# Performance work log

Hardware: AMD Instinct MI355X
Metric: run time of the kernel (lower is better)

Reference implementation:

```python
import jax, jax.numpy as jnp
import numpy as np

N = 10000       # nodes
E = 160000      # edges
D_IN = 256      # in_channels (node feature dim)
H1, C = 8, 32   # conv1: 8 heads x 32 -> 256; conv2: 1 head x 32
MSG = 128       # msg_dim
TD = 128        # time encoder out_channels
ED = MSG + TD   # edge_dim = 256
HC1 = H1 * C    # 256


def _lin(key, shape, scale=0.05):
    return jax.random.normal(key, shape, dtype=jnp.float32) * scale


def setup_inputs() -> dict:
    key = jax.random.key(0)
    ks = jax.random.split(key, 32)
    inp = {}
    inp["x"] = jax.random.normal(ks[0], (N, D_IN), dtype=jnp.float32)
    inp["last_update"] = jax.random.uniform(ks[1], (N,), jnp.float32, 0.0, 1000.0)
    inp["edge_index"] = jax.random.randint(ks[2], (2, E), 0, N)
    inp["t"] = jax.random.uniform(ks[3], (E,), jnp.float32, 0.0, 1000.0)
    inp["msg"] = jax.random.normal(ks[4], (E, MSG), dtype=jnp.float32)
    # TimeEncoder: Linear(1, TD) then cos
    inp["time_w"] = _lin(ks[5], (TD, 1), 0.1)
    inp["time_b"] = jnp.zeros((TD,), jnp.float32)
    # conv1 (TransformerConv in=256, heads=8, per-head 32, edge_dim=256, concat=True)
    inp["Wq1"] = _lin(ks[6], (D_IN, HC1)); inp["bq1"] = jnp.zeros((HC1,), jnp.float32)
    inp["Wk1"] = _lin(ks[7], (D_IN, HC1)); inp["bk1"] = jnp.zeros((HC1,), jnp.float32)
    inp["Wv1"] = _lin(ks[8], (D_IN, HC1)); inp["bv1"] = jnp.zeros((HC1,), jnp.float32)
    inp["We1"] = _lin(ks[9], (ED, HC1))   # lin_edge has no bias in PyG
    inp["Ws1"] = _lin(ks[10], (D_IN, HC1)); inp["bs1"] = jnp.zeros((HC1,), jnp.float32)
    # conv2 (in=256, heads=1, per-head 32, concat=False)
    inp["Wq2"] = _lin(ks[11], (HC1, C)); inp["bq2"] = jnp.zeros((C,), jnp.float32)
    inp["Wk2"] = _lin(ks[12], (HC1, C)); inp["bk2"] = jnp.zeros((C,), jnp.float32)
    inp["Wv2"] = _lin(ks[13], (HC1, C)); inp["bv2"] = jnp.zeros((C,), jnp.float32)
    inp["We2"] = _lin(ks[14], (ED, C))
    inp["Ws2"] = _lin(ks[15], (HC1, C)); inp["bs2"] = jnp.zeros((C,), jnp.float32)
    return inp


def transformer_conv(x, src, dst, edge_attr, Wq, bq, Wk, bk, Wv, bv, We, Ws, bs, heads, ch, concat):
    n = x.shape[0]
    q = (x @ Wq + bq).reshape(n, heads, ch)
    k = (x @ Wk + bk).reshape(n, heads, ch)
    v = (x @ Wv + bv).reshape(n, heads, ch)
    e = (edge_attr @ We).reshape(-1, heads, ch)       # [E,H,C]
    ke = k[src] + e                                    # key_j + edge
    ve = v[src] + e                                    # value_j + edge
    alpha = jnp.einsum('ehc,ehc->eh', q[dst], ke) / jnp.sqrt(jnp.float32(ch))
    # segment softmax over incoming edges of each destination node
    amax = jax.ops.segment_max(alpha, dst, num_segments=n)   # -inf for empty segs
    ex = jnp.exp(alpha - amax[dst])
    den = jax.ops.segment_sum(ex, dst, num_segments=n)
    attn = ex / (den[dst] + 1e-16)                     # [E,H]
    out = jax.ops.segment_sum(attn[:, :, None] * ve, dst, num_segments=n)  # [N,H,C]
    out = out.reshape(n, heads * ch) if concat else out.mean(axis=1)
    return out + (x @ Ws + bs)                         # root skip connection


def reference(x, last_update, edge_index, t, msg, time_w, time_b,
              Wq1, bq1, Wk1, bk1, Wv1, bv1, We1, Ws1, bs1,
              Wq2, bq2, Wk2, bk2, Wv2, bv2, We2, Ws2, bs2):
    src, dst = edge_index[0], edge_index[1]
    rel_t = last_update[src] - t                       # [E]
    rel_t_enc = jnp.cos(rel_t[:, None] * time_w[:, 0][None, :] + time_b)  # [E,TD]
    edge_attr = jnp.concatenate([rel_t_enc, msg], axis=-1)                # [E,ED]
    h = jax.nn.relu(transformer_conv(x, src, dst, edge_attr,
                                     Wq1, bq1, Wk1, bk1, Wv1, bv1, We1, Ws1, bs1,
                                     H1, C, True))
    out = jax.nn.relu(transformer_conv(h, src, dst, edge_attr,
                                       Wq2, bq2, Wk2, bk2, Wv2, bv2, We2, Ws2, bs2,
                                       1, C, False))
    return out
```

## Files before the change

kernel.cpp:

```cpp
#include <hip/hip_runtime.h>
#include <math.h>

#define N_NODES 10000
#define N_EDGES 160000
#define RT1 157
#define RTE 2500
#define CONVX_T (RT1 * 64 * 32)
#define MAXSEG 16
#define SEGSTRIDE 576

static inline int ceildiv(int a, int b) { return (a + b - 1) / b; }

typedef float f32x4 __attribute__((ext_vector_type(4)));
typedef short bf16x8 __attribute__((ext_vector_type(8)));

__device__ __forceinline__ unsigned short f2bf(float f) {
  unsigned int u = __builtin_bit_cast(unsigned int, f);
  u += 0x7FFFu + ((u >> 16) & 1u);
  return (unsigned short)(u >> 16);
}
__device__ __forceinline__ float bf2f(unsigned short h) {
  unsigned int u = ((unsigned int)h) << 16;
  return __builtin_bit_cast(float, u);
}

__global__ void count_kernel(const int* __restrict__ dstp, int* __restrict__ deg, int E) {
  for (int i = blockIdx.x * blockDim.x + threadIdx.x; i < E; i += gridDim.x * blockDim.x)
    atomicAdd(&deg[dstp[i]], 1);
}

__global__ void scan_kernel(const int* __restrict__ deg, int* __restrict__ rowptr, int n) {
  __shared__ int part[1024];
  const int tid = threadIdx.x;
  const int CHK = 10;
  int base = tid * CHK;
  int loc[CHK];
  int s = 0;
#pragma unroll
  for (int j = 0; j < CHK; ++j) {
    int idx = base + j;
    int v = (idx < n) ? deg[idx] : 0;
    loc[j] = s; s += v;
  }
  part[tid] = s;
  __syncthreads();
  for (int off = 1; off < 1024; off <<= 1) {
    int y = (tid >= off) ? part[tid - off] : 0;
    __syncthreads();
    part[tid] += y;
    __syncthreads();
  }
  int pre = tid ? part[tid - 1] : 0;
#pragma unroll
  for (int j = 0; j < CHK; ++j) {
    int idx = base + j;
    if (idx < n) rowptr[idx] = pre + loc[j];
  }
  if (tid == 1023) rowptr[n] = part[1023];
}

__global__ void scatter_kernel(const float* __restrict__ lu, const float* __restrict__ tt,
                               const int* __restrict__ srcp, const int* __restrict__ dstp,
                               const int* __restrict__ rowptr, int* __restrict__ fill,
                               int* __restrict__ srcs, int* __restrict__ dsts,
                               int* __restrict__ eidA, float* __restrict__ rel_s, int E) {
  for (int e = blockIdx.x * blockDim.x + threadIdx.x; e < E; e += gridDim.x * blockDim.x) {
    int d = dstp[e], s = srcp[e];
    int pos = atomicAdd(&fill[d], 1);
    int slot = rowptr[d] + pos;
    srcs[slot] = s;
    dsts[slot] = d;
    eidA[slot] = e;
    rel_s[slot] = lu[s] - tt[e];
  }
}

__device__ __forceinline__ void wstore(const float* __restrict__ W, unsigned short* __restrict__ out,
                                       int Nin, int n_off, int NFtot, int k, int c) {
  int gc = n_off + c;
  int ks=k>>5, kg=(k>>3)&3, j=k&7, nf=gc>>4, ic=gc&15;
  out[(size_t)(ks*NFtot+nf)*512 + (ic+16*kg)*8 + j] = f2bf(W[(size_t)k*Nin + c]);
}

__global__ void conv_all_kernel(const float* __restrict__ x, unsigned short* __restrict__ xa,
                                const float* Wq1, const float* Wk1, const float* Wv1, const float* Ws1,
                                const float* We1, const float* Wq2, const float* Wk2, const float* Wv2,
                                const float* Ws2, const float* We2,
                                const float* bq1, const float* bk1, const float* bv1, const float* bs1,
                                const float* bq2, const float* bk2, const float* bv2, const float* bs2,
                                unsigned short* W1f, unsigned short* We1f, unsigned short* W2f,
                                unsigned short* We2f, float* bcat1, float* bcat2) {
  int t0 = blockIdx.x * blockDim.x + threadIdx.x;
  if (t0 < CONVX_T) {
    int i = t0 >> 5, k8 = t0 & 31;
    union { uint4 q; unsigned short s[8]; } u;
    if (i < N_NODES) {
      const float4* px = (const float4*)(x + (size_t)i * 256 + k8 * 8);
      float4 f0 = px[0], f1 = px[1];
      u.s[0]=f2bf(f0.x); u.s[1]=f2bf(f0.y); u.s[2]=f2bf(f0.z); u.s[3]=f2bf(f0.w);
      u.s[4]=f2bf(f1.x); u.s[5]=f2bf(f1.y); u.s[6]=f2bf(f1.z); u.s[7]=f2bf(f1.w);
    } else {
      u.q = make_uint4(0,0,0,0);
    }
    int rt=i>>6, rf=(i>>4)&3, ir=i&15, ks=k8>>2, kg=k8&3;
    *(uint4*)&xa[(size_t)rt*16384 + ks*2048 + rf*512 + (ir+16*kg)*8] = u.q;
    return;
  }
  int t = t0 - CONVX_T;
  if (t < 262144) {
    int w = t >> 16, r = t & 65535, k = r >> 8, c = r & 255;
    const float* W = (w == 0) ? Wq1 : (w == 1) ? Wk1 : (w == 2) ? Wv1 : Ws1;
    wstore(W, W1f, 256, w * 256, 64, k, c);
  } else if (t < 327680) {
    int r = t - 262144, k = r >> 8, c = r & 255;
    wstore(We1, We1f, 256, 0, 16, k, c);
  } else if (t < 360448) {
    int r = t - 327680, w = r >> 13, r2 = r & 8191, k = r2 >> 5, c = r2 & 31;
    const float* W = (w == 0) ? Wq2 : (w == 1) ? Wk2 : (w == 2) ? Wv2 : Ws2;
    wstore(W, W2f, 32, w * 32, 8, k, c);
  } else if (t < 368640) {
    int r = t - 360448, k = r >> 5, c = r & 31;
    wstore(We2, We2f, 32, 0, 4, k, c);
  } else if (t < 369792) {
    int r = t - 368640;
    if (r < 1024) {
      const float* b = (r < 256) ? bq1 : (r < 512) ? bk1 : (r < 768) ? bv1 : bs1;
      bcat1[r] = b[r & 255];
    } else {
      int r2 = r - 1024;
      const float* b = (r2 < 32) ? bq2 : (r2 < 64) ? bk2 : (r2 < 96) ? bv2 : bs2;
      bcat2[r2] = b[r2 & 31];
    }
  }
}

__global__ __launch_bounds__(512, 4)
void node1_gemm(const unsigned short* __restrict__ xa, const unsigned short* __restrict__ W1f,
                const float* __restrict__ bcat1, float* __restrict__ qf,
                unsigned short* __restrict__ kvb, float* __restrict__ sf) {
  __shared__ char ldsraw[32768];
  uint4* lds4 = (uint4*)ldsraw;
  const int tid = threadIdx.x;
  const int wid = tid >> 6, lane = tid & 63;
  const int fr0 = (lane >> 4) * 4;
  const int fc0 = lane & 15;
  const int rt0 = blockIdx.x % RT1;
  const int y = blockIdx.x / RT1;
  const int phase = rt0 & 7;

#pragma unroll
  for (int s = 0; s < 4; ++s)
    lds4[tid + s * 512] = *(const uint4*)(xa + (size_t)rt0 * 16384 + (size_t)(tid + s * 512) * 8);
  __syncthreads();

  f32x4 acc[4][2];
#pragma unroll
  for (int i = 0; i < 4; ++i)
#pragma unroll
    for (int j = 0; j < 2; ++j) acc[i][j] = (f32x4){0.f, 0.f, 0.f, 0.f};

  bf16x8 aN0, aN1, aN2, aN3, bN0, bN1;
  {
    const int ks = phase;
    aN0 = *(const bf16x8*)&lds4[ks * 256 + 0 * 64 + lane];
    aN1 = *(const bf16x8*)&lds4[ks * 256 + 1 * 64 + lane];
    aN2 = *(const bf16x8*)&lds4[ks * 256 + 2 * 64 + lane];
    aN3 = *(const bf16x8*)&lds4[ks * 256 + 3 * 64 + lane];
    bN0 = *(const bf16x8*)(W1f + ((size_t)(ks * 64 + y * 16 + wid * 2 + 0)) * 512 + (size_t)lane * 8);
    bN1 = *(const bf16x8*)(W1f + ((size_t)(ks * 64 + y * 16 + wid * 2 + 1)) * 512 + (size_t)lane * 8);
  }
#pragma unroll
  for (int ksi = 0; ksi < 8; ++ksi) {
    bf16x8 aC0 = aN0, aC1 = aN1, aC2 = aN2, aC3 = aN3;
    bf16x8 bC0 = bN0, bC1 = bN1;
    if (ksi < 7) {
      const int ks2 = (ksi + 1) ^ phase;
      aN0 = *(const bf16x8*)&lds4[ks2 * 256 + 0 * 64 + lane];
      aN1 = *(const bf16x8*)&lds4[ks2 * 256 + 1 * 64 + lane];
      aN2 = *(const bf16x8*)&lds4[ks2 * 256 + 2 * 64 + lane];
      aN3 = *(const bf16x8*)&lds4[ks2 * 256 + 3 * 64 + lane];
      bN0 = *(const bf16x8*)(W1f + ((size_t)(ks2 * 64 + y * 16 + wid * 2 + 0)) * 512 + (size_t)lane * 8);
      bN1 = *(const bf16x8*)(W1f + ((size_t)(ks2 * 64 + y * 16 + wid * 2 + 1)) * 512 + (size_t)lane * 8);
    }
    acc[0][0] = __builtin_amdgcn_mfma_f32_16x16x32_bf16(aC0, bC0, acc[0][0], 0, 0, 0);
    acc[1][0] = __builtin_amdgcn_mfma_f32_16x16x32_bf16(aC1, bC0, acc[1][0], 0, 0, 0);
    acc[2][0] = __builtin_amdgcn_mfma_f32_16x16x32_bf16(aC2, bC0, acc[2][0], 0, 0, 0);
    acc[3][0] = __builtin_amdgcn_mfma_f32_16x16x32_bf16(aC3, bC0, acc[3][0], 0, 0, 0);
    acc[0][1] = __builtin_amdgcn_mfma_f32_16x16x32_bf16(aC0, bC1, acc[0][1], 0, 0, 0);
    acc[1][1] = __builtin_amdgcn_mfma_f32_16x16x32_bf16(aC1, bC1, acc[1][1], 0, 0, 0);
    acc[2][1] = __builtin_amdgcn_mfma_f32_16x16x32_bf16(aC2, bC1, acc[2][1], 0, 0, 0);
    acc[3][1] = __builtin_amdgcn_mfma_f32_16x16x32_bf16(aC3, bC1, acc[3][1], 0, 0, 0);
  }

  bool bf16path;
  void* dstp_; int cstr_, dc0_, bcol0_;
  if (y == 0)      { bf16path = false; dstp_ = qf;  cstr_ = 256; dc0_ = 0;   bcol0_ = 0; }
  else if (y == 1) { bf16path = true;  dstp_ = kvb; cstr_ = 512; dc0_ = 0;   bcol0_ = 256; }
  else if (y == 2) { bf16path = true;  dstp_ = kvb; cstr_ = 512; dc0_ = 256; bcol0_ = 512; }
  else             { bf16path = false; dstp_ = sf;  cstr_ = 256; dc0_ = 0;   bcol0_ = 768; }
  if (!bf16path) {
    float* dst = (float*)dstp_;
    const int row0 = rt0 * 64 + fr0;
#pragma unroll
    for (int cf = 0; cf < 2; ++cf) {
      int c = wid * 32 + cf * 16 + fc0;
      float bv = bcat1[bcol0_ + c];
#pragma unroll
      for (int rf = 0; rf < 4; ++rf) {
#pragma unroll
        for (int j = 0; j < 4; ++j) {
          int r = row0 + rf * 16 + j;
          if (r < N_NODES) dst[(size_t)r * cstr_ + c] = acc[rf][cf][j] + bv;
        }
      }
    }
  } else {
    __syncthreads();
    unsigned short* cl = (unsigned short*)ldsraw;
    unsigned short* dst = (unsigned short*)dstp_;
    for (int pass = 0; pass < 4; ++pass) {
      if ((wid >> 1) == pass) {
#pragma unroll
        for (int cf = 0; cf < 2; ++cf) {
          int c = (wid & 1) * 32 + cf * 16 + fc0;
          float bv = bcat1[bcol0_ + pass * 64 + c];
#pragma unroll
          for (int rf = 0; rf < 4; ++rf)
#pragma unroll
            for (int j = 0; j < 4; ++j)
              cl[(fr0 + rf * 16 + j) * 72 + c] = f2bf(acc[rf][cf][j] + bv);
        }
      }
      __syncthreads();
      {
        int row = tid >> 3, cc = (tid & 7) * 8;
        int gr = rt0 * 64 + row;
        if (gr < N_NODES)
          *(uint4*)&dst[(size_t)gr * cstr_ + dc0_ + pass * 64 + cc] = *(const uint4*)&cl[row * 72 + cc];
      }
      __syncthreads();
    }
  }
}

__global__ __launch_bounds__(512, 4)
void edge_fused(const float* __restrict__ qf, const unsigned short* __restrict__ kvb,
                const unsigned short* __restrict__ We1f, const unsigned short* __restrict__ We2f,
                char* __restrict__ segrec, unsigned short* __restrict__ e2b,
                const float* __restrict__ rel_s, const float* __restrict__ tw,
                const float* __restrict__ tb, const float* __restrict__ msg,
                const int* __restrict__ eidA, const int* __restrict__ srcsA,
                const int* __restrict__ dstsA, const int* __restrict__ rowptr) {
  __shared__ char ldsraw[38912];
  uint4* lds4 = (uint4*)ldsraw;
  unsigned short* e1t = (unsigned short*)ldsraw;
  int* dseg     = (int*)(ldsraw + 33280);
  int* sseg     = (int*)(ldsraw + 33536);
  unsigned short* cl2 = (unsigned short*)(ldsraw + 33792);

  const int tid = threadIdx.x;
  const int wid = tid >> 6, lane = tid & 63;
  const int bx = blockIdx.x;
  const int fr0 = (lane >> 4) * 4;
  const int fc0 = lane & 15;
  const int rt0 = bx;
  const int phase = bx & 7;

  {
    const int rem = tid & 255;
    const int ksh = tid >> 8;
    const int arf = rem >> 6, ar2 = rem & 63, air = ar2 & 15, akg = ar2 >> 4;
    const int slot = rt0 * 64 + arf * 16 + air;
    float rl = rel_s[slot];
    int eorg = eidA[slot];
#pragma unroll
    for (int s = 0; s < 2; ++s) {
      int ks = ksh + s * 2;
      int k8 = ks * 4 + akg;
      const float4* twp = (const float4*)(tw + k8 * 8);
      const float4* tbp = (const float4*)(tb + k8 * 8);
      float4 w0 = twp[0], w1 = twp[1], b0 = tbp[0], b1 = tbp[1];
      union { uint4 q; unsigned short us[8]; } u;
      u.us[0]=f2bf(__cosf(rl*w0.x+b0.x)); u.us[1]=f2bf(__cosf(rl*w0.y+b0.y));
      u.us[2]=f2bf(__cosf(rl*w0.z+b0.z)); u.us[3]=f2bf(__cosf(rl*w0.w+b0.w));
      u.us[4]=f2bf(__cosf(rl*w1.x+b1.x)); u.us[5]=f2bf(__cosf(rl*w1.y+b1.y));
      u.us[6]=f2bf(__cosf(rl*w1.z+b1.z)); u.us[7]=f2bf(__cosf(rl*w1.w+b1.w));
      lds4[ks * 256 + rem] = u.q;
    }
#pragma unroll
    for (int s = 0; s < 2; ++s) {
      int ks = 4 + ksh + s * 2;
      int k8 = ks * 4 + akg;
      const float4* pm = (const float4*)(msg + (size_t)eorg * 128 + (size_t)(k8 - 16) * 8);
      float4 f0 = pm[0], f1 = pm[1];
      union { uint4 q; unsigned short us[8]; } u;
      u.us[0]=f2bf(f0.x); u.us[1]=f2bf(f0.y); u.us[2]=f2bf(f0.z); u.us[3]=f2bf(f0.w);
      u.us[4]=f2bf(f1.x); u.us[5]=f2bf(f1.y); u.us[6]=f2bf(f1.z); u.us[7]=f2bf(f1.w);
      lds4[ks * 256 + rem] = u.q;
    }
  }
  __syncthreads();

  f32x4 acc[4][2];
  f32x4 acc2[4];
#pragma unroll
  for (int i = 0; i < 4; ++i) {
    acc2[i] = (f32x4){0.f, 0.f, 0.f, 0.f};
#pragma unroll
    for (int j = 0; j < 2; ++j) acc[i][j] = (f32x4){0.f, 0.f, 0.f, 0.f};
  }

  bf16x8 aN0, aN1, aN2, aN3, bN0, bN1, b2N;
  {
    const int ks = phase;
    aN0 = *(const bf16x8*)&lds4[ks * 256 + 0 * 64 + lane];
    aN1 = *(const bf16x8*)&lds4[ks * 256 + 1 * 64 + lane];
    aN2 = *(const bf16x8*)&lds4[ks * 256 + 2 * 64 + lane];
    aN3 = *(const bf16x8*)&lds4[ks * 256 + 3 * 64 + lane];
    bN0 = *(const bf16x8*)(We1f + ((size_t)(ks * 16 + wid * 2 + 0)) * 512 + (size_t)lane * 8);
    bN1 = *(const bf16x8*)(We1f + ((size_t)(ks * 16 + wid * 2 + 1)) * 512 + (size_t)lane * 8);
    b2N = 0;
    if (wid < 2) b2N = *(const bf16x8*)(We2f + ((size_t)(ks * 4 + wid)) * 512 + (size_t)lane * 8);
  }
#pragma unroll
  for (int ksi = 0; ksi < 8; ++ksi) {
    bf16x8 aC0 = aN0, aC1 = aN1, aC2 = aN2, aC3 = aN3;
    bf16x8 bC0 = bN0, bC1 = bN1, b2C = b2N;
    if (ksi < 7) {
      const int ks2 = (ksi + 1) ^ phase;
      aN0 = *(const bf16x8*)&lds4[ks2 * 256 + 0 * 64 + lane];
      aN1 = *(const bf16x8*)&lds4[ks2 * 256 + 1 * 64 + lane];
      aN2 = *(const bf16x8*)&lds4[ks2 * 256 + 2 * 64 + lane];
      aN3 = *(const bf16x8*)&lds4[ks2 * 256 + 3 * 64 + lane];
      bN0 = *(const bf16x8*)(We1f + ((size_t)(ks2 * 16 + wid * 2 + 0)) * 512 + (size_t)lane * 8);
      bN1 = *(const bf16x8*)(We1f + ((size_t)(ks2 * 16 + wid * 2 + 1)) * 512 + (size_t)lane * 8);
      if (wid < 2) b2N = *(const bf16x8*)(We2f + ((size_t)(ks2 * 4 + wid)) * 512 + (size_t)lane * 8);
    }
    acc[0][0] = __builtin_amdgcn_mfma_f32_16x16x32_bf16(aC0, bC0, acc[0][0], 0, 0, 0);
    acc[1][0] = __builtin_amdgcn_mfma_f32_16x16x32_bf16(aC1, bC0, acc[1][0], 0, 0, 0);
    acc[2][0] = __builtin_amdgcn_mfma_f32_16x16x32_bf16(aC2, bC0, acc[2][0], 0, 0, 0);
    acc[3][0] = __builtin_amdgcn_mfma_f32_16x16x32_bf16(aC3, bC0, acc[3][0], 0, 0, 0);
    acc[0][1] = __builtin_amdgcn_mfma_f32_16x16x32_bf16(aC0, bC1, acc[0][1], 0, 0, 0);
    acc[1][1] = __builtin_amdgcn_mfma_f32_16x16x32_bf16(aC1, bC1, acc[1][1], 0, 0, 0);
    acc[2][1] = __builtin_amdgcn_mfma_f32_16x16x32_bf16(aC2, bC1, acc[2][1], 0, 0, 0);
    acc[3][1] = __builtin_amdgcn_mfma_f32_16x16x32_bf16(aC3, bC1, acc[3][1], 0, 0, 0);
    if (wid < 2) {
      acc2[0] = __builtin_amdgcn_mfma_f32_16x16x32_bf16(aC0, b2C, acc2[0], 0, 0, 0);
      acc2[1] = __builtin_amdgcn_mfma_f32_16x16x32_bf16(aC1, b2C, acc2[1], 0, 0, 0);
      acc2[2] = __builtin_amdgcn_mfma_f32_16x16x32_bf16(aC2, b2C, acc2[2], 0, 0, 0);
      acc2[3] = __builtin_amdgcn_mfma_f32_16x16x32_bf16(aC3, b2C, acc2[3], 0, 0, 0);
    }
  }

  __syncthreads();
  if (tid < 64) {
    dseg[tid] = dstsA[rt0 * 64 + tid];
    sseg[tid] = srcsA[rt0 * 64 + tid];
  }
#pragma unroll
  for (int cf = 0; cf < 2; ++cf)
#pragma unroll
    for (int rf = 0; rf < 4; ++rf)
#pragma unroll
      for (int j = 0; j < 4; ++j)
        e1t[(fr0 + rf * 16 + j) * 260 + wid * 32 + cf * 16 + fc0] = f2bf(acc[rf][cf][j]);
  if (wid < 2) {
#pragma unroll
    for (int rf = 0; rf < 4; ++rf)
#pragma unroll
      for (int j = 0; j < 4; ++j)
        cl2[(fr0 + rf * 16 + j) * 40 + wid * 16 + fc0] = f2bf(acc2[rf][j]);
  }
  __syncthreads();

  if (tid < 256) {
    int row = tid >> 2, cc = (tid & 3) * 8;
    *(uint4*)&e2b[(size_t)(rt0 * 64 + row) * 32 + cc] = *(const uint4*)&cl2[row * 40 + cc];
  }

  {
    const int base = wid * 8;
    const int rgj = bx * 8 + wid;
    int d8[8], s8[8];
#pragma unroll
    for (int t = 0; t < 8; ++t) { d8[t] = dseg[base + t]; s8[t] = sseg[base + t]; }

    float4 q8[8]; ushort4 k8[8], e8[8];
#pragma unroll
    for (int t = 0; t < 8; ++t) {
      q8[t] = *(const float4*)&qf[(size_t)d8[t] * 256 + lane * 4];
      k8[t] = *(const ushort4*)&kvb[(size_t)s8[t] * 512 + lane * 4];
      e8[t] = *(const ushort4*)&e1t[(base + t) * 260 + lane * 4];
    }
    float sc[8];
#pragma unroll
    for (int t = 0; t < 8; ++t) {
      float p = q8[t].x * (bf2f(k8[t].x) + bf2f(e8[t].x))
              + q8[t].y * (bf2f(k8[t].y) + bf2f(e8[t].y))
              + q8[t].z * (bf2f(k8[t].z) + bf2f(e8[t].z))
              + q8[t].w * (bf2f(k8[t].w) + bf2f(e8[t].w));
      p += __shfl_xor(p, 1); p += __shfl_xor(p, 2); p += __shfl_xor(p, 4);
      sc[t] = p * 0.17677669529663687f;
    }
    ushort4 v8[8];
#pragma unroll
    for (int t = 0; t < 8; ++t)
      v8[t] = *(const ushort4*)&kvb[(size_t)s8[t] * 512 + 256 + lane * 4];

    float m8[8], w8[8];
#pragma unroll
    for (int t = 0; t < 8; ++t) {
      float mm = sc[t];
#pragma unroll
      for (int u = 0; u < 8; ++u)
        if (d8[u] == d8[t]) mm = fmaxf(mm, sc[u]);
      m8[t] = mm;
      w8[t] = __expf(sc[t] - mm);
    }
#pragma unroll
    for (int t = 0; t < 8; ++t) {
      bool first = (t == 0) || (d8[t - 1] != d8[t]);
      if (first && (lane & 7) == 0) {
        float den = 0.f;
#pragma unroll
        for (int u = 0; u < 8; ++u)
          if (d8[u] == d8[t]) den += w8[u];
        int j = rgj - (rowptr[d8[t]] >> 3);
        if (j < MAXSEG) {
          float* rec = (float*)(segrec + ((size_t)d8[t] * MAXSEG + j) * SEGSTRIDE);
          rec[128 + (lane >> 3)] = m8[t];
          rec[136 + (lane >> 3)] = den;
        }
      }
    }
    f32x4 pacc = (f32x4){0.f, 0.f, 0.f, 0.f};
    int cur = d8[0];
#pragma unroll
    for (int t = 0; t < 8; ++t) {
      if (d8[t] != cur) {
        int j = rgj - (rowptr[cur] >> 3);
        if (j < MAXSEG) {
          unsigned short* pp = (unsigned short*)(segrec + ((size_t)cur * MAXSEG + j) * SEGSTRIDE);
          ushort4 o;
          o.x = f2bf(pacc[0]); o.y = f2bf(pacc[1]); o.z = f2bf(pacc[2]); o.w = f2bf(pacc[3]);
          *(ushort4*)&pp[lane * 4] = o;
        }
        pacc = (f32x4){0.f, 0.f, 0.f, 0.f};
        cur = d8[t];
      }
      pacc[0] += w8[t] * (bf2f(v8[t].x) + bf2f(e8[t].x));
      pacc[1] += w8[t] * (bf2f(v8[t].y) + bf2f(e8[t].y));
      pacc[2] += w8[t] * (bf2f(v8[t].z) + bf2f(e8[t].z));
      pacc[3] += w8[t] * (bf2f(v8[t].w) + bf2f(e8[t].w));
    }
    {
      int j = rgj - (rowptr[cur] >> 3);
      if (j < MAXSEG) {
        unsigned short* pp = (unsigned short*)(segrec + ((size_t)cur * MAXSEG + j) * SEGSTRIDE);
        ushort4 o;
        o.x = f2bf(pacc[0]); o.y = f2bf(pacc[1]); o.z = f2bf(pacc[2]); o.w = f2bf(pacc[3]);
        *(ushort4*)&pp[lane * 4] = o;
      }
    }
  }
}

__global__ __launch_bounds__(64)
void merge_kernel(const char* __restrict__ segrec, const int* __restrict__ rowptr,
                  const float* __restrict__ sf, unsigned short* __restrict__ ha) {
  const int n = blockIdx.x;
  const int lane = threadIdx.x;
  const int beg = rowptr[n], end = rowptr[n + 1];
  const float4 sk = *(const float4*)&sf[(size_t)n * 256 + lane * 4];
  float o0, o1, o2, o3;
  if (beg == end) {
    o0 = sk.x; o1 = sk.y; o2 = sk.z; o3 = sk.w;
  } else {
    const int h = lane >> 3;
    int s0 = beg >> 3, s1 = (end - 1) >> 3;
    int span = s1 - s0 + 1; if (span > MAXSEG) span = MAXSEG;
    float M = -INFINITY;
    for (int j = 0; j < span; ++j) {
      const float* rec = (const float*)(segrec + ((size_t)n * MAXSEG + j) * SEGSTRIDE);
      M = fmaxf(M, rec[128 + h]);
    }
    float den = 0.f;
    f32x4 num = (f32x4){0.f, 0.f, 0.f, 0.f};
    for (int j = 0; j < span; ++j) {
      const float* rec = (const float*)(segrec + ((size_t)n * MAXSEG + j) * SEGSTRIDE);
      float sc = __expf(rec[128 + h] - M);
      den += sc * rec[136 + h];
      ushort4 p4 = *(const ushort4*)((const unsigned short*)rec + lane * 4);
      num[0] += sc * bf2f(p4.x); num[1] += sc * bf2f(p4.y);
      num[2] += sc * bf2f(p4.z); num[3] += sc * bf2f(p4.w);
    }
    const float inv = 1.f / (den + 1e-16f);
    o0 = num[0] * inv + sk.x; o1 = num[1] * inv + sk.y;
    o2 = num[2] * inv + sk.z; o3 = num[3] * inv + sk.w;
  }
  o0 = fmaxf(o0, 0.f); o1 = fmaxf(o1, 0.f); o2 = fmaxf(o2, 0.f); o3 = fmaxf(o3, 0.f);
  int rt = n >> 6, rf = (n >> 4) & 3, ir = n & 15;
  int h2 = lane >> 3;
  int kg = (lane & 7) >> 1, jj = 4 * (lane & 1);
  ushort4 w4;
  w4.x = f2bf(o0); w4.y = f2bf(o1); w4.z = f2bf(o2); w4.w = f2bf(o3);
  *(ushort4*)&ha[(size_t)rt * 16384 + h2 * 2048 + rf * 512 + (ir + 16 * kg) * 8 + jj] = w4;
}

__global__ __launch_bounds__(256)
void gemm_node2(const unsigned short* __restrict__ ha, const unsigned short* __restrict__ W2f,
                const float* __restrict__ bcat2, float* __restrict__ qkvs2) {
  const int tid = threadIdx.x;
  const int wid = tid >> 6, lane = tid & 63;
  const int wr = wid >> 1, wc = wid & 1;
  const int rt0 = blockIdx.x * 2;
  int rtA = rt0 + wr;
  if (rtA >= RT1) rtA = RT1 - 1;

  f32x4 acc[4][4];
#pragma unroll
  for (int i = 0; i < 4; ++i)
#pragma unroll
    for (int j = 0; j < 4; ++j) acc[i][j] = (f32x4){0.f, 0.f, 0.f, 0.f};

#pragma unroll
  for (int ks = 0; ks < 8; ++ks) {
    bf16x8 a[4], b[4];
#pragma unroll
    for (int rf = 0; rf < 4; ++rf)
      a[rf] = *(const bf16x8*)(ha + (size_t)rtA * 16384 + (size_t)ks * 2048 + (size_t)(rf * 64 + lane) * 8);
#pragma unroll
    for (int cf = 0; cf < 4; ++cf)
      b[cf] = *(const bf16x8*)(W2f + ((size_t)(ks * 8 + wc * 4 + cf)) * 512 + (size_t)lane * 8);
#pragma unroll
    for (int rf = 0; rf < 4; ++rf)
#pragma unroll
      for (int cf = 0; cf < 4; ++cf)
        acc[rf][cf] = __builtin_amdgcn_mfma_f32_16x16x32_bf16(a[rf], b[cf], acc[rf][cf], 0, 0, 0);
  }

  const int row0 = (rt0 + wr) * 64 + ((lane >> 4) * 4);
  const int cb2 = wc * 64 + (lane & 15);
#pragma unroll
  for (int cf = 0; cf < 4; ++cf) {
    int c = cb2 + cf * 16;
    float bv = bcat2[c];
#pragma unroll
    for (int rf = 0; rf < 4; ++rf) {
#pragma unroll
      for (int j = 0; j < 4; ++j) {
        int r = row0 + rf * 16 + j;
        if (r < N_NODES) qkvs2[(size_t)r * 128 + c] = acc[rf][cf][j] + bv;
      }
    }
  }
}

__global__ __launch_bounds__(64)
void attn2_kernel(const float* __restrict__ qkvs2, const unsigned short* __restrict__ e2b,
                  const int* __restrict__ srcs, const int* __restrict__ rowptr,
                  float* __restrict__ outp) {
  const int n = blockIdx.x;
  const int tid = threadIdx.x;
  const int c = tid & 31;
  const int beg = rowptr[n], end = rowptr[n + 1];
  const float qv = qkvs2[(size_t)n * 128 + c];

  float m0=-INFINITY,d0=0,x0=0;
  float m1=-INFINITY,d1=0,x1=0;
  float m2=-INFINITY,d2=0,x2=0;
  float m3=-INFINITY,d3=0,x3=0;

  auto step = [&](int i, float& m, float& d, float& a) {
    const int s = srcs[i];
    const float ev = bf2f(e2b[(size_t)i * 32 + c]);
    float p = qv * (qkvs2[(size_t)s * 128 + 32 + c] + ev);
    const float v = qkvs2[(size_t)s * 128 + 64 + c] + ev;
#pragma unroll
    for (int off = 16; off; off >>= 1) p += __shfl_xor(p, off);
    p *= 0.17677669529663687f;
    const float mn = fmaxf(m, p);
    const float sc = __expf(m - mn), w = __expf(p - mn);
    d = d * sc + w; a = a * sc + w * v; m = mn;
  };

  int i = beg;
  for (; i + 3 < end; i += 4) {
    step(i, m0, d0, x0);
    step(i + 1, m1, d1, x1);
    step(i + 2, m2, d2, x2);
    step(i + 3, m3, d3, x3);
  }
  for (; i < end; ++i) step(i, m0, d0, x0);

  auto merge = [&](float& m, float& d, float& a, float mB, float dB, float b) {
    if (mB == -INFINITY) return;
    const float M = fmaxf(m, mB);
    const float sA = __expf(m - M), sB = __expf(mB - M);
    d = d * sA + dB * sB; a = a * sA + b * sB; m = M;
  };
  merge(m0, d0, x0, m1, d1, x1);
  merge(m2, d2, x2, m3, d3, x3);
  merge(m0, d0, x0, m2, d2, x2);

  if (tid < 32) {
    float o = x0 / (d0 + 1e-16f) + qkvs2[(size_t)n * 128 + 96 + c];
    outp[(size_t)n * 32 + c] = fmaxf(o, 0.f);
  }
}

extern "C" void kernel_launch(void* const* d_in, const int* in_sizes, int n_in,
                              void* d_out, int out_size, void* d_ws, size_t ws_size,
                              hipStream_t stream) {
  const float* x   = (const float*)d_in[0];
  const float* lu  = (const float*)d_in[1];
  const int*   ei  = (const int*)d_in[2];
  const float* tt  = (const float*)d_in[3];
  const float* msg = (const float*)d_in[4];
  const float* tw  = (const float*)d_in[5];
  const float* tb  = (const float*)d_in[6];
  const float* Wq1 = (const float*)d_in[7];  const float* bq1 = (const float*)d_in[8];
  const float* Wk1 = (const float*)d_in[9];  const float* bk1 = (const float*)d_in[10];
  const float* Wv1 = (const float*)d_in[11]; const float* bv1 = (const float*)d_in[12];
  const float* We1 = (const float*)d_in[13];
  const float* Ws1 = (const float*)d_in[14]; const float* bs1 = (const float*)d_in[15];
  const float* Wq2 = (const float*)d_in[16]; const float* bq2 = (const float*)d_in[17];
  const float* Wk2 = (const float*)d_in[18]; const float* bk2 = (const float*)d_in[19];
  const float* Wv2 = (const float*)d_in[20]; const float* bv2 = (const float*)d_in[21];
  const float* We2 = (const float*)d_in[22];
  const float* Ws2 = (const float*)d_in[23]; const float* bs2 = (const float*)d_in[24];

  const int* srcp = ei;
  const int* dstp = ei + N_EDGES;

  char* p = (char*)d_ws;
  auto alloc = [&](size_t bytes) -> char* {
    char* r = p;
    p += (bytes + 255) & ~(size_t)255;
    return r;
  };
  int*   deg     = (int*)alloc((size_t)N_NODES * 4);
  int*   fill    = (int*)alloc((size_t)N_NODES * 4);
  int*   rowptr  = (int*)alloc((size_t)(N_NODES + 1) * 4);
  int*   srcs    = (int*)alloc((size_t)N_EDGES * 4);
  int*   dsts    = (int*)alloc((size_t)N_EDGES * 4);
  int*   eidA    = (int*)alloc((size_t)N_EDGES * 4);
  float* rel_s   = (float*)alloc((size_t)N_EDGES * 4);
  unsigned short* xa   = (unsigned short*)alloc((size_t)RT1 * 32768);
  unsigned short* W1f  = (unsigned short*)alloc((size_t)8 * 64 * 1024);
  unsigned short* We1f = (unsigned short*)alloc((size_t)8 * 16 * 1024);
  unsigned short* W2f  = (unsigned short*)alloc((size_t)8 * 8 * 1024);
  unsigned short* We2f = (unsigned short*)alloc((size_t)8 * 4 * 1024);
  float* bcat1  = (float*)alloc(1024 * 4);
  float* bcat2  = (float*)alloc(128 * 4);
  float* qf     = (float*)alloc((size_t)N_NODES * 256 * 4);
  unsigned short* kvb = (unsigned short*)alloc((size_t)N_NODES * 512 * 2);
  float* sf     = (float*)alloc((size_t)N_NODES * 256 * 4);
  char*  segrec = (char*)alloc((size_t)N_NODES * MAXSEG * SEGSTRIDE);
  unsigned short* ha  = (unsigned short*)alloc((size_t)RT1 * 32768);
  float* qkvs2  = (float*)alloc((size_t)N_NODES * 128 * 4);
  unsigned short* e2b = (unsigned short*)alloc((size_t)N_EDGES * 32 * 2);
  float* outp   = (float*)d_out;

  hipMemsetAsync(deg, 0, (size_t)N_NODES * 4, stream);
  hipMemsetAsync(fill, 0, (size_t)N_NODES * 4, stream);
  hipMemsetAsync(ha + (size_t)(RT1 - 1) * 16384, 0, 32768, stream);

  count_kernel<<<625, 256, 0, stream>>>(dstp, deg, N_EDGES);
  scan_kernel<<<1, 1024, 0, stream>>>(deg, rowptr, N_NODES);
  scatter_kernel<<<625, 256, 0, stream>>>(lu, tt, srcp, dstp, rowptr, fill,
                                          srcs, dsts, eidA, rel_s, N_EDGES);

  conv_all_kernel<<<ceildiv(CONVX_T + 369792, 256), 256, 0, stream>>>(
      x, xa, Wq1, Wk1, Wv1, Ws1, We1, Wq2, Wk2, Wv2, Ws2, We2,
      bq1, bk1, bv1, bs1, bq2, bk2, bv2, bs2,
      W1f, We1f, W2f, We2f, bcat1, bcat2);

  node1_gemm<<<RT1 * 4, 512, 0, stream>>>(xa, W1f, bcat1, qf, kvb, sf);

  edge_fused<<<RTE, 512, 0, stream>>>(
      qf, kvb, We1f, We2f, segrec, e2b,
      rel_s, tw, tb, msg, eidA, srcs, dsts, rowptr);

  merge_kernel<<<N_NODES, 64, 0, stream>>>(segrec, rowptr, sf, ha);
  gemm_node2<<<ceildiv(RT1, 2), 256, 0, stream>>>(ha, W2f, bcat2, qkvs2);
  attn2_kernel<<<N_NODES, 64, 0, stream>>>(qkvs2, e2b, srcs, rowptr, outp);
}
```

Measured before the change: 170.8 us.

## Fuse merge into node2 GEMM, overlap msg loads with cos compute, batch attn2 nodes

The separate merge_kernel and gemm_node2 are fused into node2_fused. It merges segment records per node and writes the bf16 A-tile straight into LDS, removing the global ha buffer, its memset and one launch. In edge_fused the msg loads are issued early and the first half of the K loop runs on the cos features, with the msg half converted and stored to LDS afterwards; this hides global load latency but adds a barrier and drops the phase-rotated K order. attn2 now packs four nodes per 256-thread block instead of one per 64-thread block. The fused node2 kernel has only 157 blocks with a serial per-thread merge loop, so it may run with low parallelism.

```diff
diff --git a/kernel.cpp b/kernel.cpp
--- a/kernel.cpp
+++ b/kernel.cpp
@@ -264,15 +264,23 @@
   const int fr0 = (lane >> 4) * 4;
   const int fc0 = lane & 15;
   const int rt0 = bx;
-  const int phase = bx & 7;
-
+
+  const int rem = tid & 255;
+  const int ksh = tid >> 8;
+  float4 mA0, mA1, mB0, mB1;
   {
-    const int rem = tid & 255;
-    const int ksh = tid >> 8;
     const int arf = rem >> 6, ar2 = rem & 63, air = ar2 & 15, akg = ar2 >> 4;
     const int slot = rt0 * 64 + arf * 16 + air;
+    int eorg = eidA[slot];
+    const float4* pmA = (const float4*)(msg + (size_t)eorg * 128 + (size_t)(ksh * 4 + akg) * 8);
+    mA0 = pmA[0]; mA1 = pmA[1];
+    const float4* pmB = (const float4*)(msg + (size_t)eorg * 128 + (size_t)((2 + ksh) * 4 + akg) * 8);
+    mB0 = pmB[0]; mB1 = pmB[1];
+    if (tid < 64) {
+      dseg[tid] = dstsA[rt0 * 64 + tid];
+      sseg[tid] = srcsA[rt0 * 64 + tid];
+    }
     float rl = rel_s[slot];
-    int eorg = eidA[slot];
 #pragma unroll
     for (int s = 0; s < 2; ++s) {
       int ks = ksh + s * 2;
@@ -287,17 +295,6 @@
       u.us[6]=f2bf(__cosf(rl*w1.z+b1.z)); u.us[7]=f2bf(__cosf(rl*w1.w+b1.w));
       lds4[ks * 256 + rem] = u.q;
     }
-#pragma unroll
-    for (int s = 0; s < 2; ++s) {
-      int ks = 4 + ksh + s * 2;
-      int k8 = ks * 4 + akg;
-      const float4* pm = (const float4*)(msg + (size_t)eorg * 128 + (size_t)(k8 - 16) * 8);
-      float4 f0 = pm[0], f1 = pm[1];
-      union { uint4 q; unsigned short us[8]; } u;
-      u.us[0]=f2bf(f0.x); u.us[1]=f2bf(f0.y); u.us[2]=f2bf(f0.z); u.us[3]=f2bf(f0.w);
-      u.us[4]=f2bf(f1.x); u.us[5]=f2bf(f1.y); u.us[6]=f2bf(f1.z); u.us[7]=f2bf(f1.w);
-      lds4[ks * 256 + rem] = u.q;
-    }
   }
   __syncthreads();
 
@@ -310,53 +307,82 @@
     for (int j = 0; j < 2; ++j) acc[i][j] = (f32x4){0.f, 0.f, 0.f, 0.f};
   }
 
-  bf16x8 aN0, aN1, aN2, aN3, bN0, bN1, b2N;
+  bf16x8 bN0, bN1, b2N;
+  bN0 = *(const bf16x8*)(We1f + ((size_t)(0 * 16 + wid * 2 + 0)) * 512 + (size_t)lane * 8);
+  bN1 = *(const bf16x8*)(We1f + ((size_t)(0 * 16 + wid * 2 + 1)) * 512 + (size_t)lane * 8);
+  b2N = 0;
+  if (wid < 2) b2N = *(const bf16x8*)(We2f + ((size_t)(0 * 4 + wid)) * 512 + (size_t)lane * 8);
+#pragma unroll
+  for (int ks = 0; ks < 4; ++ks) {
+    bf16x8 bC0 = bN0, bC1 = bN1, b2C = b2N;
+    if (ks < 3) {
+      bN0 = *(const bf16x8*)(We1f + ((size_t)((ks + 1) * 16 + wid * 2 + 0)) * 512 + (size_t)lane * 8);
+      bN1 = *(const bf16x8*)(We1f + ((size_t)((ks + 1) * 16 + wid * 2 + 1)) * 512 + (size_t)lane * 8);
+      if (wid < 2) b2N = *(const bf16x8*)(We2f + ((size_t)((ks + 1) * 4 + wid)) * 512 + (size_t)lane * 8);
+    }
+    bf16x8 a0 = *(const bf16x8*)&lds4[ks * 256 + 0 * 64 + lane];
+    bf16x8 a1 = *(const bf16x8*)&lds4[ks * 256 + 1 * 64 + lane];
+    bf16x8 a2 = *(const bf16x8*)&lds4[ks * 256 + 2 * 64 + lane];
+    bf16x8 a3 = *(const bf16x8*)&lds4[ks * 256 + 3 * 64 + lane];
+    acc[0][0] = __builtin_amdgcn_mfma_f32_16x16x32_bf16(a0, bC0, acc[0][0], 0, 0, 0);
+    acc[1][0] = __builtin_amdgcn_mfma_f32_16x16x32_bf16(a1, bC0, acc[1][0], 0, 0, 0);
+    acc[2][0] = __builtin_amdgcn_mfma_f32_16x16x32_bf16(a2, bC0, acc[2][0], 0, 0, 0);
+    acc[3][0] = __builtin_amdgcn_mfma_f32_16x16x32_bf16(a3, bC0, acc[3][0], 0, 0, 0);
+    acc[0][1] = __builtin_amdgcn_mfma_f32_16x16x32_bf16(a0, bC1, acc[0][1], 0, 0, 0);
+    acc[1][1] = __builtin_amdgcn_mfma_f32_16x16x32_bf16(a1, bC1, acc[1][1], 0, 0, 0);
+    acc[2][1] = __builtin_amdgcn_mfma_f32_16x16x32_bf16(a2, bC1, acc[2][1], 0, 0, 0);
+    acc[3][1] = __builtin_amdgcn_mfma_f32_16x16x32_bf16(a3, bC1, acc[3][1], 0, 0, 0);
+    if (wid < 2) {
+      acc2[0] = __builtin_amdgcn_mfma_f32_16x16x32_bf16(a0, b2C, acc2[0], 0, 0, 0);
+      acc2[1] = __builtin_amdgcn_mfma_f32_16x16x32_bf16(a1, b2C, acc2[1], 0, 0, 0);
+      acc2[2] = __builtin_amdgcn_mfma_f32_16x16x32_bf16(a2, b2C, acc2[2], 0, 0, 0);
+      acc2[3] = __builtin_amdgcn_mfma_f32_16x16x32_bf16(a3, b2C, acc2[3], 0, 0, 0);
+    }
+  }
+
+  bN0 = *(const bf16x8*)(We1f + ((size_t)(4 * 16 + wid * 2 + 0)) * 512 + (size_t)lane * 8);
+  bN1 = *(const bf16x8*)(We1f + ((size_t)(4 * 16 + wid * 2 + 1)) * 512 + (size_t)lane * 8);
+  if (wid < 2) b2N = *(const bf16x8*)(We2f + ((size_t)(4 * 4 + wid)) * 512 + (size_t)lane * 8);
   {
-    const int ks = phase;
-    aN0 = *(const bf16x8*)&lds4[ks * 256 + 0 * 64 + lane];
-    aN1 = *(const bf16x8*)&lds4[ks * 256 + 1 * 64 + lane];
-    aN2 = *(const bf16x8*)&lds4[ks * 256 + 2 * 64 + lane];
-    aN3 = *(const bf16x8*)&lds4[ks * 256 + 3 * 64 + lane];
-    bN0 = *(const bf16x8*)(We1f + ((size_t)(ks * 16 + wid * 2 + 0)) * 512 + (size_t)lane * 8);
-    bN1 = *(const bf16x8*)(We1f + ((size_t)(ks * 16 + wid * 2 + 1)) * 512 + (size_t)lane * 8);
-    b2N = 0;
-    if (wid < 2) b2N = *(const bf16x8*)(We2f + ((size_t)(ks * 4 + wid)) * 512 + (size_t)lane * 8);
-  }
-#pragma unroll
-  for (int ksi = 0; ksi < 8; ++ksi) {
-    bf16x8 aC0 = aN0, aC1 = aN1, aC2 = aN2, aC3 = aN3;
+    union { uint4 q; unsigned short us[8]; } u;
+    u.us[0]=f2bf(mA0.x); u.us[1]=f2bf(mA0.y); u.us[2]=f2bf(mA0.z); u.us[3]=f2bf(mA0.w);
+    u.us[4]=f2bf(mA1.x); u.us[5]=f2bf(mA1.y); u.us[6]=f2bf(mA1.z); u.us[7]=f2bf(mA1.w);
+    lds4[(4 + ksh) * 256 + rem] = u.q;
+    u.us[0]=f2bf(mB0.x); u.us[1]=f2bf(mB0.y); u.us[2]=f2bf(mB0.z); u.us[3]=f2bf(mB0.w);
+    u.us[4]=f2bf(mB1.x); u.us[5]=f2bf(mB1.y); u.us[6]=f2bf(mB1.z); u.us[7]=f2bf(mB1.w);
+    lds4[(6 + ksh) * 256 + rem] = u.q;
+  }
+  __syncthreads();
+
+#pragma unroll
+  for (int ks = 4; ks < 8; ++ks) {
     bf16x8 bC0 = bN0, bC1 = bN1, b2C = b2N;
-    if (ksi < 7) {
-      const int ks2 = (ksi + 1) ^ phase;
-      aN0 = *(const bf16x8*)&lds4[ks2 * 256 + 0 * 64 + lane];
-      aN1 = *(const bf16x8*)&lds4[ks2 * 256 + 1 * 64 + lane];
-      aN2 = *(const bf16x8*)&lds4[ks2 * 256 + 2 * 64 + lane];
-      aN3 = *(const bf16x8*)&lds4[ks2 * 256 + 3 * 64 + lane];
-      bN0 = *(const bf16x8*)(We1f + ((size_t)(ks2 * 16 + wid * 2 + 0)) * 512 + (size_t)lane * 8);
-      bN1 = *(const bf16x8*)(We1f + ((size_t)(ks2 * 16 + wid * 2 + 1)) * 512 + (size_t)lane * 8);
-      if (wid < 2) b2N = *(const bf16x8*)(We2f + ((size_t)(ks2 * 4 + wid)) * 512 + (size_t)lane * 8);
-    }
-    acc[0][0] = __builtin_amdgcn_mfma_f32_16x16x32_bf16(aC0, bC0, acc[0][0], 0, 0, 0);
-    acc[1][0] = __builtin_amdgcn_mfma_f32_16x16x32_bf16(aC1, bC0, acc[1][0], 0, 0, 0);
-    acc[2][0] = __builtin_amdgcn_mfma_f32_16x16x32_bf16(aC2, bC0, acc[2][0], 0, 0, 0);
-    acc[3][0] = __builtin_amdgcn_mfma_f32_16x16x32_bf16(aC3, bC0, acc[3][0], 0, 0, 0);
-    acc[0][1] = __builtin_amdgcn_mfma_f32_16x16x32_bf16(aC0, bC1, acc[0][1], 0, 0, 0);
-    acc[1][1] = __builtin_amdgcn_mfma_f32_16x16x32_bf16(aC1, bC1, acc[1][1], 0, 0, 0);
-    acc[2][1] = __builtin_amdgcn_mfma_f32_16x16x32_bf16(aC2, bC1, acc[2][1], 0, 0, 0);
-    acc[3][1] = __builtin_amdgcn_mfma_f32_16x16x32_bf16(aC3, bC1, acc[3][1], 0, 0, 0);
+    if (ks < 7) {
+      bN0 = *(const bf16x8*)(We1f + ((size_t)((ks + 1) * 16 + wid * 2 + 0)) * 512 + (size_t)lane * 8);
+      bN1 = *(const bf16x8*)(We1f + ((size_t)((ks + 1) * 16 + wid * 2 + 1)) * 512 + (size_t)lane * 8);
+      if (wid < 2) b2N = *(const bf16x8*)(We2f + ((size_t)((ks + 1) * 4 + wid)) * 512 + (size_t)lane * 8);
+    }
+    bf16x8 a0 = *(const bf16x8*)&lds4[ks * 256 + 0 * 64 + lane];
+    bf16x8 a1 = *(const bf16x8*)&lds4[ks * 256 + 1 * 64 + lane];
+    bf16x8 a2 = *(const bf16x8*)&lds4[ks * 256 + 2 * 64 + lane];
+    bf16x8 a3 = *(const bf16x8*)&lds4[ks * 256 + 3 * 64 + lane];
+    acc[0][0] = __builtin_amdgcn_mfma_f32_16x16x32_bf16(a0, bC0, acc[0][0], 0, 0, 0);
+    acc[1][0] = __builtin_amdgcn_mfma_f32_16x16x32_bf16(a1, bC0, acc[1][0], 0, 0, 0);
+    acc[2][0] = __builtin_amdgcn_mfma_f32_16x16x32_bf16(a2, bC0, acc[2][0], 0, 0, 0);
+    acc[3][0] = __builtin_amdgcn_mfma_f32_16x16x32_bf16(a3, bC0, acc[3][0], 0, 0, 0);
+    acc[0][1] = __builtin_amdgcn_mfma_f32_16x16x32_bf16(a0, bC1, acc[0][1], 0, 0, 0);
+    acc[1][1] = __builtin_amdgcn_mfma_f32_16x16x32_bf16(a1, bC1, acc[1][1], 0, 0, 0);
+    acc[2][1] = __builtin_amdgcn_mfma_f32_16x16x32_bf16(a2, bC1, acc[2][1], 0, 0, 0);
+    acc[3][1] = __builtin_amdgcn_mfma_f32_16x16x32_bf16(a3, bC1, acc[3][1], 0, 0, 0);
     if (wid < 2) {
-      acc2[0] = __builtin_amdgcn_mfma_f32_16x16x32_bf16(aC0, b2C, acc2[0], 0, 0, 0);
-      acc2[1] = __builtin_amdgcn_mfma_f32_16x16x32_bf16(aC1, b2C, acc2[1], 0, 0, 0);
-      acc2[2] = __builtin_amdgcn_mfma_f32_16x16x32_bf16(aC2, b2C, acc2[2], 0, 0, 0);
-      acc2[3] = __builtin_amdgcn_mfma_f32_16x16x32_bf16(aC3, b2C, acc2[3], 0, 0, 0);
+      acc2[0] = __builtin_amdgcn_mfma_f32_16x16x32_bf16(a0, b2C, acc2[0], 0, 0, 0);
+      acc2[1] = __builtin_amdgcn_mfma_f32_16x16x32_bf16(a1, b2C, acc2[1], 0, 0, 0);
+      acc2[2] = __builtin_amdgcn_mfma_f32_16x16x32_bf16(a2, b2C, acc2[2], 0, 0, 0);
+      acc2[3] = __builtin_amdgcn_mfma_f32_16x16x32_bf16(a3, b2C, acc2[3], 0, 0, 0);
     }
   }
 
   __syncthreads();
-  if (tid < 64) {
-    dseg[tid] = dstsA[rt0 * 64 + tid];
-    sseg[tid] = srcsA[rt0 * 64 + tid];
-  }
 #pragma unroll
   for (int cf = 0; cf < 2; ++cf)
 #pragma unroll
@@ -465,84 +491,116 @@
   }
 }
 
-__global__ __launch_bounds__(64)
-void merge_kernel(const char* __restrict__ segrec, const int* __restrict__ rowptr,
-                  const float* __restrict__ sf, unsigned short* __restrict__ ha) {
-  const int n = blockIdx.x;
-  const int lane = threadIdx.x;
-  const int beg = rowptr[n], end = rowptr[n + 1];
-  const float4 sk = *(const float4*)&sf[(size_t)n * 256 + lane * 4];
-  float o0, o1, o2, o3;
-  if (beg == end) {
-    o0 = sk.x; o1 = sk.y; o2 = sk.z; o3 = sk.w;
-  } else {
-    const int h = lane >> 3;
-    int s0 = beg >> 3, s1 = (end - 1) >> 3;
-    int span = s1 - s0 + 1; if (span > MAXSEG) span = MAXSEG;
-    float M = -INFINITY;
-    for (int j = 0; j < span; ++j) {
-      const float* rec = (const float*)(segrec + ((size_t)n * MAXSEG + j) * SEGSTRIDE);
-      M = fmaxf(M, rec[128 + h]);
-    }
-    float den = 0.f;
-    f32x4 num = (f32x4){0.f, 0.f, 0.f, 0.f};
-    for (int j = 0; j < span; ++j) {
-      const float* rec = (const float*)(segrec + ((size_t)n * MAXSEG + j) * SEGSTRIDE);
-      float sc = __expf(rec[128 + h] - M);
-      den += sc * rec[136 + h];
-      ushort4 p4 = *(const ushort4*)((const unsigned short*)rec + lane * 4);
-      num[0] += sc * bf2f(p4.x); num[1] += sc * bf2f(p4.y);
-      num[2] += sc * bf2f(p4.z); num[3] += sc * bf2f(p4.w);
-    }
-    const float inv = 1.f / (den + 1e-16f);
-    o0 = num[0] * inv + sk.x; o1 = num[1] * inv + sk.y;
-    o2 = num[2] * inv + sk.z; o3 = num[3] * inv + sk.w;
-  }
-  o0 = fmaxf(o0, 0.f); o1 = fmaxf(o1, 0.f); o2 = fmaxf(o2, 0.f); o3 = fmaxf(o3, 0.f);
-  int rt = n >> 6, rf = (n >> 4) & 3, ir = n & 15;
-  int h2 = lane >> 3;
-  int kg = (lane & 7) >> 1, jj = 4 * (lane & 1);
-  ushort4 w4;
-  w4.x = f2bf(o0); w4.y = f2bf(o1); w4.z = f2bf(o2); w4.w = f2bf(o3);
-  *(ushort4*)&ha[(size_t)rt * 16384 + h2 * 2048 + rf * 512 + (ir + 16 * kg) * 8 + jj] = w4;
-}
-
 __global__ __launch_bounds__(256)
-void gemm_node2(const unsigned short* __restrict__ ha, const unsigned short* __restrict__ W2f,
-                const float* __restrict__ bcat2, float* __restrict__ qkvs2) {
+void node2_fused(const char* __restrict__ segrec, const int* __restrict__ rowptr,
+                 const float* __restrict__ sf, const unsigned short* __restrict__ W2f,
+                 const float* __restrict__ bcat2, float* __restrict__ qkvs2) {
+  __shared__ unsigned short haL[8 * 2048];
   const int tid = threadIdx.x;
   const int wid = tid >> 6, lane = tid & 63;
-  const int wr = wid >> 1, wc = wid & 1;
-  const int rt0 = blockIdx.x * 2;
-  int rtA = rt0 + wr;
-  if (rtA >= RT1) rtA = RT1 - 1;
-
-  f32x4 acc[4][4];
+  const int rt0 = blockIdx.x;
+
+  {
+    const int nl = tid >> 2;
+    const int n = rt0 * 64 + nl;
+    const int cb = (tid & 3) * 64;
+    const int rf = (nl >> 4) & 3, ir = nl & 15;
+    if (n < N_NODES) {
+      const int beg = rowptr[n], end = rowptr[n + 1];
+      int s0 = 0, span = 0;
+      if (beg < end) {
+        s0 = beg >> 3;
+        span = ((end - 1) >> 3) - s0 + 1;
+        if (span > MAXSEG) span = MAXSEG;
+      }
+#pragma unroll
+      for (int cc = 0; cc < 4; ++cc) {
+        const int c0 = cb + cc * 16;
+        const int h = c0 >> 5;
+        float o[16];
+        if (span == 0) {
+#pragma unroll
+          for (int q = 0; q < 16; ++q) o[q] = 0.f;
+        } else {
+          float M = -INFINITY;
+          for (int j = 0; j < span; ++j) {
+            const float* rec = (const float*)(segrec + ((size_t)n * MAXSEG + j) * SEGSTRIDE);
+            M = fmaxf(M, rec[128 + h]);
+          }
+          float den = 0.f;
+#pragma unroll
+          for (int q = 0; q < 16; ++q) o[q] = 0.f;
+          for (int j = 0; j < span; ++j) {
+            const float* rec = (const float*)(segrec + ((size_t)n * MAXSEG + j) * SEGSTRIDE);
+            float scj = __expf(rec[128 + h] - M);
+            den += scj * rec[136 + h];
+            const unsigned short* pp = (const unsigned short*)rec;
+#pragma unroll
+            for (int q4 = 0; q4 < 4; ++q4) {
+              ushort4 p4 = *(const ushort4*)&pp[c0 + q4 * 4];
+              o[q4*4+0] += scj * bf2f(p4.x); o[q4*4+1] += scj * bf2f(p4.y);
+              o[q4*4+2] += scj * bf2f(p4.z); o[q4*4+3] += scj * bf2f(p4.w);
+            }
+          }
+          const float inv = 1.f / (den + 1e-16f);
+#pragma unroll
+          for (int q = 0; q < 16; ++q) o[q] *= inv;
+        }
+#pragma unroll
+        for (int q4 = 0; q4 < 4; ++q4) {
+          const int c = c0 + q4 * 4;
+          float4 sk = *(const float4*)&sf[(size_t)n * 256 + c];
+          ushort4 w4;
+          w4.x = f2bf(fmaxf(o[q4*4+0] + sk.x, 0.f));
+          w4.y = f2bf(fmaxf(o[q4*4+1] + sk.y, 0.f));
+          w4.z = f2bf(fmaxf(o[q4*4+2] + sk.z, 0.f));
+          w4.w = f2bf(fmaxf(o[q4*4+3] + sk.w, 0.f));
+          int ks = c >> 5, kg = (c >> 3) & 3, j = c & 7;
+          *(ushort4*)&haL[ks * 2048 + rf * 512 + (ir + 16 * kg) * 8 + j] = w4;
+        }
+      }
+    } else {
+#pragma unroll
+      for (int cc = 0; cc < 4; ++cc) {
+        const int c0 = cb + cc * 16;
+#pragma unroll
+        for (int q4 = 0; q4 < 4; ++q4) {
+          const int c = c0 + q4 * 4;
+          int ks = c >> 5, kg = (c >> 3) & 3, j = c & 7;
+          ushort4 z; z.x = z.y = z.z = z.w = 0;
+          *(ushort4*)&haL[ks * 2048 + rf * 512 + (ir + 16 * kg) * 8 + j] = z;
+        }
+      }
+    }
+  }
+  __syncthreads();
+
+  f32x4 acc[4][2];
 #pragma unroll
   for (int i = 0; i < 4; ++i)
 #pragma unroll
-    for (int j = 0; j < 4; ++j) acc[i][j] = (f32x4){0.f, 0.f, 0.f, 0.f};
+    for (int j = 0; j < 2; ++j) acc[i][j] = (f32x4){0.f, 0.f, 0.f, 0.f};
 
 #pragma unroll
   for (int ks = 0; ks < 8; ++ks) {
-    bf16x8 a[4], b[4];
+    bf16x8 a[4], b[2];
 #pragma unroll
     for (int rf = 0; rf < 4; ++rf)
-      a[rf] = *(const bf16x8*)(ha + (size_t)rtA * 16384 + (size_t)ks * 2048 + (size_t)(rf * 64 + lane) * 8);
-#pragma unroll
-    for (int cf = 0; cf < 4; ++cf)
-      b[cf] = *(const bf16x8*)(W2f + ((size_t)(ks * 8 + wc * 4 + cf)) * 512 + (size_t)lane * 8);
+      a[rf] = *(const bf16x8*)&haL[ks * 2048 + (rf * 64 + lane) * 8];
+#pragma unroll
+    for (int cf = 0; cf < 2; ++cf)
+      b[cf] = *(const bf16x8*)(W2f + ((size_t)(ks * 8 + wid * 2 + cf)) * 512 + (size_t)lane * 8);
 #pragma unroll
     for (int rf = 0; rf < 4; ++rf)
 #pragma unroll
-      for (int cf = 0; cf < 4; ++cf)
+      for (int cf = 0; cf < 2; ++cf)
         acc[rf][cf] = __builtin_amdgcn_mfma_f32_16x16x32_bf16(a[rf], b[cf], acc[rf][cf], 0, 0, 0);
   }
 
-  const int row0 = (rt0 + wr) * 64 + ((lane >> 4) * 4);
-  const int cb2 = wc * 64 + (lane & 15);
-#pragma unroll
-  for (int cf = 0; cf < 4; ++cf) {
+  const int row0 = rt0 * 64 + ((lane >> 4) * 4);
+  const int cb2 = wid * 32 + (lane & 15);
+#pragma unroll
+  for (int cf = 0; cf < 2; ++cf) {
     int c = cb2 + cf * 16;
     float bv = bcat2[c];
 #pragma unroll
@@ -556,13 +614,14 @@
   }
 }
 
-__global__ __launch_bounds__(64)
+__global__ __launch_bounds__(256)
 void attn2_kernel(const float* __restrict__ qkvs2, const unsigned short* __restrict__ e2b,
                   const int* __restrict__ srcs, const int* __restrict__ rowptr,
                   float* __restrict__ outp) {
-  const int n = blockIdx.x;
-  const int tid = threadIdx.x;
-  const int c = tid & 31;
+  const int n = blockIdx.x * 4 + (threadIdx.x >> 6);
+  if (n >= N_NODES) return;
+  const int lane = threadIdx.x & 63;
+  const int c = lane & 31;
   const int beg = rowptr[n], end = rowptr[n + 1];
   const float qv = qkvs2[(size_t)n * 128 + c];
 
@@ -603,7 +662,7 @@
   merge(m2, d2, x2, m3, d3, x3);
   merge(m0, d0, x0, m2, d2, x2);
 
-  if (tid < 32) {
+  if (lane < 32) {
     float o = x0 / (d0 + 1e-16f) + qkvs2[(size_t)n * 128 + 96 + c];
     outp[(size_t)n * 32 + c] = fmaxf(o, 0.f);
   }
@@ -657,14 +716,12 @@
   unsigned short* kvb = (unsigned short*)alloc((size_t)N_NODES * 512 * 2);
   float* sf     = (float*)alloc((size_t)N_NODES * 256 * 4);
   char*  segrec = (char*)alloc((size_t)N_NODES * MAXSEG * SEGSTRIDE);
-  unsigned short* ha  = (unsigned short*)alloc((size_t)RT1 * 32768);
   float* qkvs2  = (float*)alloc((size_t)N_NODES * 128 * 4);
   unsigned short* e2b = (unsigned short*)alloc((size_t)N_EDGES * 32 * 2);
   float* outp   = (float*)d_out;
 
   hipMemsetAsync(deg, 0, (size_t)N_NODES * 4, stream);
   hipMemsetAsync(fill, 0, (size_t)N_NODES * 4, stream);
-  hipMemsetAsync(ha + (size_t)(RT1 - 1) * 16384, 0, 32768, stream);
 
   count_kernel<<<625, 256, 0, stream>>>(dstp, deg, N_EDGES);
   scan_kernel<<<1, 1024, 0, stream>>>(deg, rowptr, N_NODES);
@@ -682,7 +739,6 @@
       qf, kvb, We1f, We2f, segrec, e2b,
       rel_s, tw, tb, msg, eidA, srcs, dsts, rowptr);
 
-  merge_kernel<<<N_NODES, 64, 0, stream>>>(segrec, rowptr, sf, ha);
-  gemm_node2<<<ceildiv(RT1, 2), 256, 0, stream>>>(ha, W2f, bcat2, qkvs2);
-  attn2_kernel<<<N_NODES, 64, 0, stream>>>(qkvs2, e2b, srcs, rowptr, outp);
-}
+  node2_fused<<<RT1, 256, 0, stream>>>(segrec, rowptr, sf, W2f, bcat2, qkvs2);
+  attn2_kernel<<<ceildiv(N_NODES, 4), 256, 0, stream>>>(qkvs2, e2b, srcs, rowptr, outp);
+}
```

Measured after the change: 172.2 us. About the same (+0.9%).
